# Performance work log

Measured on AMD Instinct MI355X. Metric: run time of the kernel, lower is better.

## Reference

```python
import jax, jax.numpy as jnp
import numpy as np

B, S, E, H = 4, 2048, 1024, 16
D = E // H

def setup_inputs() -> dict:
    key = jax.random.key(0)
    ks = jax.random.split(key, 8)
    sc = lambda fan_in: 1.0 / np.sqrt(fan_in)
    return {
        "query": jax.random.normal(ks[0], (B, S, E), jnp.float32),
        "Wq": jax.random.normal(ks[1], (E, E), jnp.float32) * sc(E),
        "bq": jnp.zeros((E,), jnp.float32),
        "Wk": jax.random.normal(ks[2], (E, E), jnp.float32) * sc(E),
        "bk": jnp.zeros((E,), jnp.float32),
        "Wv": jax.random.normal(ks[3], (E, E), jnp.float32) * sc(E),
        "bv": jnp.zeros((E,), jnp.float32),
        "Wo": jax.random.normal(ks[4], (E, E), jnp.float32) * sc(E),
        "bo": jnp.zeros((E,), jnp.float32),
        "Wm1": jax.random.normal(ks[5], (E // 4, E), jnp.float32) * sc(E),
        "bm1": jnp.zeros((E // 4,), jnp.float32),
        "Wm2": jax.random.normal(ks[6], (E, E // 4), jnp.float32) * sc(E // 4),
        "bm2": jnp.zeros((E,), jnp.float32),
        "dopamine": jnp.ones((1,), jnp.float32),
        "serotonin": jnp.ones((1,), jnp.float32),
        "norepinephrine": jnp.ones((1,), jnp.float32),
        "acetylcholine": jnp.ones((1,), jnp.float32),
        "attn_scale": jnp.ones((1,), jnp.float32),
        "attn_bias": jnp.zeros((1,), jnp.float32),
    }

def reference(query, Wq, bq, Wk, bk, Wv, bv, Wo, bo,
              Wm1, bm1, Wm2, bm2,
              dopamine, serotonin, norepinephrine, acetylcholine,
              attn_scale, attn_bias):
    scale = D ** (-0.5)
    # projections (nn.Linear: y = x @ W.T + b)
    q = (query @ Wq.T + bq).reshape(B, S, H, D).transpose(0, 2, 1, 3)  # [B,H,S,D]
    k = (query @ Wk.T + bk).reshape(B, S, H, D).transpose(0, 2, 1, 3)
    v = (query @ Wv.T + bv).reshape(B, S, H, D).transpose(0, 2, 1, 3)
    scores = jnp.einsum('bhqd,bhkd->bhqk', q, k) * scale  # [B,H,S,S]
    probs = jax.nn.softmax(scores, axis=-1)
    attn = jnp.einsum('bhqk,bhkd->bhqd', probs, v)  # [B,H,S,D]
    # neuromodulation: MLP on query, summed scalar-weighted effects / 4
    mod = jax.nn.relu(query @ Wm1.T + bm1) @ Wm2.T + bm2  # [B,S,E]
    nm_gain = (dopamine + serotonin + norepinephrine + acetylcholine) / 4.0  # [1]
    neuromod = (mod * nm_gain).reshape(B, S, H, D).transpose(0, 2, 1, 3)  # [B,H,S,D]
    attn = (attn * attn_scale + attn_bias) * (1.0 + neuromod)
    attn = attn.transpose(0, 2, 1, 3).reshape(B, S, E)
    return attn @ Wo.T + bo
```

## Files before the change

kernel.cpp:

```cpp
#include <hip/hip_runtime.h>
#include <hip/hip_bf16.h>
#include <cstdint>

#define PB 4
#define PS 2048
#define PE 1024
#define PH 16
#define PD 64
#define PM (PB * PS)

typedef __attribute__((ext_vector_type(8))) _Float16 half8;
typedef __attribute__((ext_vector_type(4))) float f32x4;

#define MFMAH __builtin_amdgcn_mfma_f32_16x16x32_f16

#define GLOAD_LDS(gp, lp) __builtin_amdgcn_global_load_lds(                    \
    (const __attribute__((address_space(1))) void*)(gp),                       \
    (__attribute__((address_space(3))) void*)(lp), 16, 0, 0)

#if __has_builtin(__builtin_amdgcn_exp2f)
#define FAST_EXP2 1
#define QSC (0.125f * 1.4426950408889634f)
#define FTHR 11.5415603f
#define EXP_P(x) __builtin_amdgcn_exp2f(x)
#else
#define FAST_EXP2 0
#define QSC 0.125f
#define FTHR 8.f
#define EXP_P(x) __expf(x)
#endif

__device__ inline unsigned short h16(float x) {
    _Float16 h = (_Float16)x;
    unsigned short u;
    __builtin_memcpy(&u, &h, 2);
    return u;
}
__device__ inline unsigned pkrtz(float a, float b) {
    auto p = __builtin_amdgcn_cvt_pkrtz(a, b);
    unsigned u;
    __builtin_memcpy(&u, &p, 4);
    return u;
}

__global__ __launch_bounds__(256)
void split_all(const float* __restrict__ q,   const float* __restrict__ wq,
               const float* __restrict__ wk,  const float* __restrict__ wv,
               const float* __restrict__ wo,  const float* __restrict__ wm1,
               const float* __restrict__ wm2,
               unsigned short* qh,  unsigned short* wqh, unsigned short* wkh,
               unsigned short* wvh, unsigned short* woh,
               unsigned short* m1h, unsigned short* m2h)
{
    const int b = blockIdx.x;
    const float* src; unsigned short* dst; int base;
    if      (b <  8192) { src = q;   dst = qh;  base = 0;     }
    else if (b <  9216) { src = wq;  dst = wqh; base = 8192;  }
    else if (b < 10240) { src = wk;  dst = wkh; base = 9216;  }
    else if (b < 11264) { src = wv;  dst = wvh; base = 10240; }
    else if (b < 12288) { src = wo;  dst = woh; base = 11264; }
    else if (b < 12544) { src = wm1; dst = m1h; base = 12288; }
    else                { src = wm2; dst = m2h; base = 12544; }
    const int i = (b - base) * 256 + threadIdx.x;
    float4 f = ((const float4*)src)[i];
    ushort4 h;
    h.x = h16(f.x); h.y = h16(f.y); h.z = h16(f.z); h.w = h16(f.w);
    ((ushort4*)dst)[i] = h;
}

__global__ __launch_bounds__(512, 2)
void gemm_qkv(const unsigned short* __restrict__ Ah,
              const unsigned short* __restrict__ Wqh,
              const unsigned short* __restrict__ Wkh,
              const unsigned short* __restrict__ Wvh,
              const float* __restrict__ bq, const float* __restrict__ bk,
              const float* __restrict__ bv,
              unsigned short* __restrict__ qh16, unsigned short* __restrict__ kf,
              unsigned short* __restrict__ vtf)
{
    __shared__ int4 ldsq[8192];
    char* const lds = (char*)ldsq;
    const int K = PE;

    const int tid  = threadIdx.x;
    const int lane = tid & 63;
    const int w    = tid >> 6;
    const int lq   = lane & 15;
    const int lg   = lane >> 4;
    const int wr   = w >> 2;
    const int wc   = w & 3;
    const int m0   = blockIdx.x * 128;
    const int n0   = blockIdx.y * 128;

    const int plane = w >> 1;
    const unsigned short* const gp =
        (plane == 0) ? Ah  + (size_t)m0 * K :
        (plane == 1) ? Wqh + (size_t)n0 * K :
        (plane == 2) ? Wkh + (size_t)n0 * K :
                       Wvh + (size_t)n0 * K;
    const int pbase = plane * 16384;
    const int ch0   = (w & 1) * 8;
    const int scol8 = (((lane & 7) ^ (lane >> 3)) << 3);
    const int lrow8 = lane >> 3;

    auto ISSUE = [&](int k0, int bufn) {
        #pragma unroll
        for (int r = 0; r < 8; ++r) {
            const int c   = ch0 + r;
            const int row = c * 8 + lrow8;
            GLOAD_LDS(gp + (size_t)row * K + k0 + scol8,
                      lds + bufn * 65536 + pbase + c * 1024 + 16 * lane);
        }
    };

    f32x4 acc[3][4][2];
    #pragma unroll
    for (int o = 0; o < 3; ++o)
        #pragma unroll
        for (int mt = 0; mt < 4; ++mt)
            #pragma unroll
            for (int nt = 0; nt < 2; ++nt)
                acc[o][mt][nt] = (f32x4){0.f, 0.f, 0.f, 0.f};

    ISSUE(0, 0);
    __syncthreads();

    int buf = 0;
    for (int k0 = 0; k0 < K; k0 += 64) {
        if (k0 + 64 < K) ISSUE(k0 + 64, buf ^ 1);

        const char* const L = lds + buf * 65536;
        #pragma unroll
        for (int kh = 0; kh < 2; ++kh) {
            half8 af[4];
            #pragma unroll
            for (int mt = 0; mt < 4; ++mt) {
                const int row = 64 * wr + 16 * mt + lq;
                const int off = row * 128 + ((kh * 64 + 16 * lg) ^ ((row & 7) << 4));
                af[mt] = *(const half8*)(L + off);
            }
            #pragma unroll
            for (int o = 0; o < 3; ++o) {
                #pragma unroll
                for (int nt = 0; nt < 2; ++nt) {
                    const int row = 32 * wc + 16 * nt + lq;
                    const int off = row * 128 + ((kh * 64 + 16 * lg) ^ ((row & 7) << 4));
                    half8 bf = *(const half8*)(L + 16384 * (o + 1) + off);
                    #pragma unroll
                    for (int mt = 0; mt < 4; ++mt)
                        acc[o][mt][nt] = MFMAH(af[mt], bf, acc[o][mt][nt], 0, 0, 0);
                }
            }
        }
        __syncthreads();
        buf ^= 1;
    }

    #pragma unroll
    for (int nt = 0; nt < 2; ++nt) {
        const int n = n0 + 32 * wc + 16 * nt + lq;
        const int h = n >> 6, d = n & 63;
        const float bqv = bq[n], bkv = bk[n], bvv = bv[n];
        #pragma unroll
        for (int mt = 0; mt < 4; ++mt) {
            #pragma unroll
            for (int j = 0; j < 4; ++j) {
                const int m = m0 + 64 * wr + 16 * mt + 4 * lg + j;
                const int b = m >> 11, s = m & 2047;
                qh16[((size_t)(b * PH + h) * PS + s) * PD + d] =
                    h16((acc[0][mt][nt][j] + bqv) * QSC);
                kf[((size_t)(b * PH + h) * PS + s) * PD + d] =
                    h16(acc[1][mt][nt][j] + bkv);
                const int scol = (s & ~63) + ((mt & 1) << 5) + (lg << 3)
                               + ((mt >> 1) << 2) + j;
                vtf[((size_t)(b * PH + h) * PD + d) * PS + scol] =
                    h16(acc[2][mt][nt][j] + bvv);
            }
        }
    }
}

template<int MODE, bool RELU>
__global__ __launch_bounds__(256, 2)
void gemm_pl(const unsigned short* __restrict__ Ah,
             const unsigned short* __restrict__ Bh,
             const float* __restrict__ bias, float* __restrict__ C,
             unsigned short* __restrict__ Oh,
             int M, int N, int K,
             const float* __restrict__ attn,
             const float* __restrict__ g0, const float* __restrict__ g1,
             const float* __restrict__ g2, const float* __restrict__ g3,
             const float* __restrict__ asc, const float* __restrict__ abi)
{
    __shared__ int4 ldsq[4096];
    char* const lds = (char*)ldsq;

    const int tid  = threadIdx.x;
    const int lane = tid & 63;
    const int w    = tid >> 6;
    const int lq   = lane & 15;
    const int lg   = lane >> 4;
    const int wm   = (w >> 1) * 64;
    const int wn   = (w & 1) * 64;
    const int m0   = blockIdx.x * 128;
    const int n0   = blockIdx.y * 128;

    const unsigned short* const gp =
        (w < 2) ? Ah + (size_t)m0 * K : Bh + (size_t)n0 * K;
    const int pb    = (w < 2) ? 0 : 16384;
    const int ch0   = (w & 1) * 8;
    const int scol8 = (((lane & 7) ^ (lane >> 3)) << 3);
    const int lrow8 = lane >> 3;

    auto ISSUE = [&](int k0, int bufn) {
        #pragma unroll
        for (int r = 0; r < 8; ++r) {
            const int c   = ch0 + r;
            const int row = c * 8 + lrow8;
            GLOAD_LDS(gp + (size_t)row * K + k0 + scol8,
                      lds + bufn * 32768 + pb + c * 1024 + 16 * lane);
        }
    };

    f32x4 acc[4][4];
    #pragma unroll
    for (int mt = 0; mt < 4; ++mt)
        #pragma unroll
        for (int nt = 0; nt < 4; ++nt)
            acc[mt][nt] = (f32x4){0.f, 0.f, 0.f, 0.f};

    ISSUE(0, 0);
    __syncthreads();

    int buf = 0;
    for (int k0 = 0; k0 < K; k0 += 64) {
        if (k0 + 64 < K) ISSUE(k0 + 64, buf ^ 1);

        const char* const L = lds + buf * 32768;
        #pragma unroll
        for (int kh = 0; kh < 2; ++kh) {
            half8 af[4];
            #pragma unroll
            for (int mt = 0; mt < 4; ++mt) {
                const int row = wm + 16 * mt + lq;
                const int off = row * 128 + ((kh * 64 + 16 * lg) ^ ((row & 7) << 4));
                af[mt] = *(const half8*)(L + off);
            }
            #pragma unroll
            for (int nt = 0; nt < 4; ++nt) {
                const int row = wn + 16 * nt + lq;
                const int off = row * 128 + ((kh * 64 + 16 * lg) ^ ((row & 7) << 4));
                half8 bf = *(const half8*)(L + 16384 + off);
                #pragma unroll
                for (int mt = 0; mt < 4; ++mt)
                    acc[mt][nt] = MFMAH(af[mt], bf, acc[mt][nt], 0, 0, 0);
            }
        }
        __syncthreads();
        buf ^= 1;
    }

    float gain = 0.f, ascv = 0.f, abiv = 0.f;
    if (MODE == 6) {
        gain = 0.25f * (*g0 + *g1 + *g2 + *g3);
        ascv = *asc;
        abiv = *abi;
    }

    #pragma unroll
    for (int nt = 0; nt < 4; ++nt) {
        const int n  = n0 + wn + 16 * nt + lq;
        const float bv = bias[n];
        #pragma unroll
        for (int mt = 0; mt < 4; ++mt) {
            #pragma unroll
            for (int j = 0; j < 4; ++j) {
                const int m = m0 + wm + 16 * mt + 4 * lg + j;
                float v = acc[mt][nt][j] + bv;
                if (RELU) v = fmaxf(v, 0.f);
                if (MODE == 0) {
                    C[(size_t)m * N + n] = v;
                } else if (MODE == 5) {
                    Oh[(size_t)m * N + n] = h16(v);
                } else {
                    const int b = m >> 11, s = m & 2047;
                    const int h = n >> 6, d = n & 63;
                    const float av = attn[((size_t)(b * PH + h) * PS + s) * PD + d];
                    const float o = (av * ascv + abiv) * (1.f + v * gain);
                    Oh[(size_t)m * N + n] = h16(o);
                }
            }
        }
    }
}

typedef __attribute__((ext_vector_type(8))) short short8;
#define MFMA16 __builtin_amdgcn_mfma_f32_16x16x32_bf16
__device__ inline unsigned short bf16rn(float x) {
    unsigned u = __builtin_bit_cast(unsigned, x);
    u += 0x7FFFu + ((u >> 16) & 1u);
    return (unsigned short)(u >> 16);
}
__device__ inline float bf16tof(unsigned short h) {
    unsigned u = ((unsigned)h) << 16;
    return __builtin_bit_cast(float, u);
}
__device__ inline void split2(float x, unsigned short& h, unsigned short& l) {
    h = bf16rn(x);
    l = bf16rn(x - bf16tof(h));
}

template<int MODE, bool RELU>
__global__ __launch_bounds__(256, 2)
void gemm_nt(const float* __restrict__ A, const float* __restrict__ Bw,
             const float* __restrict__ bias, float* __restrict__ C,
             unsigned short* __restrict__ Ohi,
             int M, int N, int K,
             const float* __restrict__ attn,
             const float* __restrict__ g0, const float* __restrict__ g1,
             const float* __restrict__ g2, const float* __restrict__ g3,
             const float* __restrict__ asc, const float* __restrict__ abi)
{
    __shared__ int4 ldsq[4096];
    char* const lds = (char*)ldsq;

    const int tid  = threadIdx.x;
    const int lane = tid & 63;
    const int w    = tid >> 6;
    const int lq   = lane & 15;
    const int lg   = lane >> 4;
    const int wm   = (w >> 1) * 64;
    const int wn   = (w & 1) * 64;
    const int m0   = blockIdx.x * 128;
    const int n0   = blockIdx.y * 128;

    const int irow = tid >> 3;
    const int ic8  = (tid & 7) * 8;
    const int woff = (ic8 * 2);

    f32x4 acc[4][4];
    #pragma unroll
    for (int mt = 0; mt < 4; ++mt)
        #pragma unroll
        for (int nt = 0; nt < 4; ++nt)
            acc[mt][nt] = (f32x4){0.f, 0.f, 0.f, 0.f};

    for (int k0 = 0; k0 < K; k0 += 64) {
        #pragma unroll
        for (int mat = 0; mat < 2; ++mat) {
            const float* const src = mat ? Bw : A;
            const int rbase = mat ? n0 : m0;
            const int pbase = mat ? 32768 : 0;
            #pragma unroll
            for (int r = 0; r < 4; ++r) {
                const int row = irow + 32 * r;
                const float* p = src + (size_t)(rbase + row) * K + k0 + ic8;
                float4 f0 = *(const float4*)p;
                float4 f1 = *(const float4*)(p + 4);
                short8 vh, vl;
                {
                    unsigned short h, l;
                    split2(f0.x, h, l); vh[0] = (short)h; vl[0] = (short)l;
                    split2(f0.y, h, l); vh[1] = (short)h; vl[1] = (short)l;
                    split2(f0.z, h, l); vh[2] = (short)h; vl[2] = (short)l;
                    split2(f0.w, h, l); vh[3] = (short)h; vl[3] = (short)l;
                    split2(f1.x, h, l); vh[4] = (short)h; vl[4] = (short)l;
                    split2(f1.y, h, l); vh[5] = (short)h; vl[5] = (short)l;
                    split2(f1.z, h, l); vh[6] = (short)h; vl[6] = (short)l;
                    split2(f1.w, h, l); vh[7] = (short)h; vl[7] = (short)l;
                }
                const int off = row * 128 + (woff ^ ((row & 7) << 4));
                *(short8*)(lds + pbase + off)         = vh;
                *(short8*)(lds + pbase + 16384 + off) = vl;
            }
        }
        __syncthreads();

        #pragma unroll
        for (int kh = 0; kh < 2; ++kh) {
            short8 afh[4], afl[4];
            #pragma unroll
            for (int mt = 0; mt < 4; ++mt) {
                const int row = wm + 16 * mt + lq;
                const int off = row * 128 + ((kh * 64 + 16 * lg) ^ ((row & 7) << 4));
                afh[mt] = *(const short8*)(lds + off);
                afl[mt] = *(const short8*)(lds + 16384 + off);
            }
            #pragma unroll
            for (int nt = 0; nt < 4; ++nt) {
                const int row = wn + 16 * nt + lq;
                const int off = row * 128 + ((kh * 64 + 16 * lg) ^ ((row & 7) << 4));
                short8 bfh = *(const short8*)(lds + 32768 + off);
                short8 bfl = *(const short8*)(lds + 49152 + off);
                #pragma unroll
                for (int mt = 0; mt < 4; ++mt) {
                    acc[mt][nt] = MFMA16(afh[mt], bfh, acc[mt][nt], 0, 0, 0);
                    acc[mt][nt] = MFMA16(afh[mt], bfl, acc[mt][nt], 0, 0, 0);
                    acc[mt][nt] = MFMA16(afl[mt], bfh, acc[mt][nt], 0, 0, 0);
                }
            }
        }
        __syncthreads();
    }

    float gain = 0.f, ascv = 0.f, abiv = 0.f;
    if (MODE == 2) {
        gain = 0.25f * (*g0 + *g1 + *g2 + *g3);
        ascv = *asc;
        abiv = *abi;
    }

    #pragma unroll
    for (int nt = 0; nt < 4; ++nt) {
        const int n  = n0 + wn + 16 * nt + lq;
        const float bv = bias[n];
        #pragma unroll
        for (int mt = 0; mt < 4; ++mt) {
            #pragma unroll
            for (int j = 0; j < 4; ++j) {
                const int m = m0 + wm + 16 * mt + 4 * lg + j;
                float v = acc[mt][nt][j] + bv;
                if (RELU) v = fmaxf(v, 0.f);
                if (MODE == 0) {
                    C[(size_t)m * N + n] = v;
                } else if (MODE == 1) {
                    const int b = m >> 11, s = m & 2047;
                    const int h = n >> 6, d = n & 63;
                    Ohi[((size_t)(b * PH + h) * PS + s) * PD + d] = h16(v * QSC);
                } else if (MODE == 3) {
                    const int b = m >> 11, s = m & 2047;
                    const int h = n >> 6, d = n & 63;
                    Ohi[((size_t)(b * PH + h) * PS + s) * PD + d] = h16(v);
                } else if (MODE == 4) {
                    const int b = m >> 11;
                    const int h = n >> 6, d = n & 63;
                    const int scol = (m & 2047 & ~63) + ((mt & 1) << 5)
                                   + (lg << 3) + ((mt >> 1) << 2) + j;
                    Ohi[((size_t)(b * PH + h) * PD + d) * PS + scol] = h16(v);
                } else {
                    const int b = m >> 11, s = m & 2047;
                    const int h = n >> 6, d = n & 63;
                    const float av = attn[((size_t)(b * PH + h) * PS + s) * PD + d];
                    C[(size_t)m * N + n] = (av * ascv + abiv) * (1.f + v * gain);
                }
            }
        }
    }
}

__global__ __launch_bounds__(256, 4)
void flash_mfma(const unsigned short* __restrict__ qh16,
                const unsigned short* __restrict__ kf,
                const unsigned short* __restrict__ vtf,
                float* attn)
{
    __shared__ int4 ldsv[2048];
    char* const ldsb = (char*)ldsv;

    const int tid  = threadIdx.x;
    const int lane = tid & 63;
    const int w    = tid >> 6;
    const int lq   = lane & 15;
    const int lg   = lane >> 4;

    const int L  = blockIdx.x + (blockIdx.y << 4) + (blockIdx.z << 8);
    const int nL = ((L & 7) << 7) + (L >> 3);
    const int bh = nL >> 4;
    const int q0 = (nL & 15) * 128 + w * 32;

    const size_t kbase = (size_t)bh * PS * PD;
    const size_t vbase = (size_t)bh * PD * PS;

    const unsigned short* const gp = (w < 2) ? kf + kbase : vtf + vbase;
    const bool isK = (w < 2);
    const int ch0   = (w & 1) * 4;
    const int scol8 = (((lane & 7) ^ (lane >> 3)) << 3);
    const int lrow8 = lane >> 3;

    auto ISSUE = [&](int kt, int bufn) {
        #pragma unroll
        for (int r = 0; r < 4; ++r) {
            const int c   = ch0 + r;
            const int row = c * 8 + lrow8;
            const size_t goff = isK ? (size_t)(kt + row) * PD + scol8
                                    : (size_t)row * PS + kt + scol8;
            GLOAD_LDS(gp + goff,
                      ldsb + bufn * 16384 + (isK ? 0 : 8192) + c * 1024 + 16 * lane);
        }
    };

    const half8 onesh = {(_Float16)1.f, (_Float16)1.f, (_Float16)1.f,
                         (_Float16)1.f, (_Float16)1.f, (_Float16)1.f,
                         (_Float16)1.f, (_Float16)1.f};

    half8 qh[2][2];
    #pragma unroll
    for (int u = 0; u < 2; ++u) {
        const unsigned short* qp =
            qh16 + ((size_t)bh * PS + q0 + 16 * u + lq) * PD + 8 * lg;
        qh[u][0] = *(const half8*)(qp);
        qh[u][1] = *(const half8*)(qp + 32);
    }

    f32x4 ot[2][4];
    #pragma unroll
    for (int u = 0; u < 2; ++u)
        #pragma unroll
        for (int mt = 0; mt < 4; ++mt)
            ot[u][mt] = (f32x4){0.f, 0.f, 0.f, 0.f};
    f32x4 lacc[2] = {{0.f,0.f,0.f,0.f}, {0.f,0.f,0.f,0.f}};
    float m_run[2] = {-3.0e38f, -3.0e38f};

    ISSUE(0, 0);
    __syncthreads();

    int buf = 0;
    for (int kti = 0; kti < PS / 64; ++kti) {
        const bool pf = (kti + 1 < PS / 64);
        if (pf) ISSUE((kti + 1) * 64, buf ^ 1);

        const char* const L2 = ldsb + buf * 16384;

        f32x4 st[2][4];
        #pragma unroll
        for (int mt = 0; mt < 4; ++mt) {
            const int row = 16 * mt + lq;
            const int swz = (row & 7) << 4;
            const char* kr = L2 + row * 128;
            half8 a0 = *(const half8*)(kr + ((16 * lg) ^ swz));
            half8 a1 = *(const half8*)(kr + ((64 + 16 * lg) ^ swz));
            #pragma unroll
            for (int u = 0; u < 2; ++u) {
                f32x4 acc = {0.f, 0.f, 0.f, 0.f};
                acc = MFMAH(a0, qh[u][0], acc, 0, 0, 0);
                acc = MFMAH(a1, qh[u][1], acc, 0, 0, 0);
                st[u][mt] = acc;
            }
        }

        half8 pb[2][2];
        #pragma unroll
        for (int u = 0; u < 2; ++u) {
            float a0 = fmaxf(fmaxf(st[u][0][0], st[u][0][1]), st[u][0][2]);
            float a1 = fmaxf(fmaxf(st[u][0][3], st[u][1][0]), st[u][1][1]);
            float a2 = fmaxf(fmaxf(st[u][1][2], st[u][1][3]), st[u][2][0]);
            float a3 = fmaxf(fmaxf(st[u][2][1], st[u][2][2]), st[u][2][3]);
            float a4 = fmaxf(fmaxf(st[u][3][0], st[u][3][1]), st[u][3][2]);
            float b0 = fmaxf(fmaxf(a0, a1), a2);
            float b1 = fmaxf(fmaxf(a3, a4), st[u][3][3]);
            float pmax = fmaxf(b0, b1);
            pmax = fmaxf(pmax, __shfl_xor(pmax, 16));
            pmax = fmaxf(pmax, __shfl_xor(pmax, 32));
            if (!__all(pmax - m_run[u] <= FTHR)) {
                float mnew = fmaxf(m_run[u], pmax);
                float corr = EXP_P(m_run[u] - mnew);
                m_run[u] = mnew;
                #pragma unroll
                for (int j = 0; j < 4; ++j)
                    lacc[u][j] *= corr;
                #pragma unroll
                for (int mt = 0; mt < 4; ++mt)
                    #pragma unroll
                    for (int j = 0; j < 4; ++j)
                        ot[u][mt][j] *= corr;
            }
            #pragma unroll
            for (int mt = 0; mt < 4; ++mt)
                #pragma unroll
                for (int j = 0; j < 4; ++j)
                    st[u][mt][j] = EXP_P(st[u][mt][j] - m_run[u]);
            #pragma unroll
            for (int t = 0; t < 2; ++t) {
                unsigned w0 = pkrtz(st[u][t][0],     st[u][t][1]);
                unsigned w1 = pkrtz(st[u][t][2],     st[u][t][3]);
                unsigned w2 = pkrtz(st[u][t + 2][0], st[u][t + 2][1]);
                unsigned w3 = pkrtz(st[u][t + 2][2], st[u][t + 2][3]);
                uint4 pw = make_uint4(w0, w1, w2, w3);
                __builtin_memcpy(&pb[u][t], &pw, 16);
            }
            lacc[u] = MFMAH(onesh, pb[u][0], lacc[u], 0, 0, 0);
            lacc[u] = MFMAH(onesh, pb[u][1], lacc[u], 0, 0, 0);
        }

        #pragma unroll
        for (int t = 0; t < 2; ++t) {
            #pragma unroll
            for (int mt = 0; mt < 4; ++mt) {
                const int row = 16 * mt + lq;
                const int swz = (row & 7) << 4;
                const char* vr = L2 + 8192 + row * 128;
                half8 vv = *(const half8*)(vr + ((t * 64 + 16 * lg) ^ swz));
                #pragma unroll
                for (int u = 0; u < 2; ++u)
                    ot[u][mt] = MFMAH(vv, pb[u][t], ot[u][mt], 0, 0, 0);
            }
        }

        __syncthreads();
        buf ^= 1;
    }

    #pragma unroll
    for (int u = 0; u < 2; ++u) {
        const float inv = 1.f / lacc[u][0];
        float* op = attn + ((size_t)bh * PS + q0 + 16 * u + lq) * PD + 4 * lg;
        #pragma unroll
        for (int mt = 0; mt < 4; ++mt) {
            float4 o;
            o.x = ot[u][mt][0] * inv; o.y = ot[u][mt][1] * inv;
            o.z = ot[u][mt][2] * inv; o.w = ot[u][mt][3] * inv;
            *(float4*)(op + 16 * mt) = o;
        }
    }
}

extern "C" void kernel_launch(void* const* d_in, const int* in_sizes, int n_in,
                              void* d_out, int out_size, void* d_ws, size_t ws_size,
                              hipStream_t stream)
{
    const float* query = (const float*)d_in[0];
    const float* Wq  = (const float*)d_in[1];  const float* bq  = (const float*)d_in[2];
    const float* Wk  = (const float*)d_in[3];  const float* bk  = (const float*)d_in[4];
    const float* Wv  = (const float*)d_in[5];  const float* bv  = (const float*)d_in[6];
    const float* Wo  = (const float*)d_in[7];  const float* bo  = (const float*)d_in[8];
    const float* Wm1 = (const float*)d_in[9];  const float* bm1 = (const float*)d_in[10];
    const float* Wm2 = (const float*)d_in[11]; const float* bm2 = (const float*)d_in[12];
    const float* dop = (const float*)d_in[13];
    const float* ser = (const float*)d_in[14];
    const float* nor = (const float*)d_in[15];
    const float* ach = (const float*)d_in[16];
    const float* asc = (const float*)d_in[17];
    const float* abi = (const float*)d_in[18];
    float* out = (float*)d_out;

    char* wsb = (char*)d_ws;
    float*          attnb = (float*)wsb;
    unsigned short* kf    = (unsigned short*)(wsb + (32u << 20));
    unsigned short* vtf   = (unsigned short*)(wsb + (48u << 20));

    dim3 blk(256);
    const bool presplit = (ws_size >= 161480704ull);

    if (presplit) {
        unsigned short* h1h   = (unsigned short*)(wsb + (64u << 20));
        unsigned short* afh   = (unsigned short*)(wsb + (72u << 20));
        unsigned short* qh16  = (unsigned short*)(wsb + (88u << 20));
        unsigned short* qh    = (unsigned short*)(wsb + (104u << 20));
        unsigned short* wqh   = (unsigned short*)(wsb + (136u << 20));
        unsigned short* wkh   = (unsigned short*)(wsb + (138u << 20));
        unsigned short* wvh   = (unsigned short*)(wsb + (140u << 20));
        unsigned short* woh   = (unsigned short*)(wsb + (142u << 20));
        unsigned short* m1h   = (unsigned short*)(wsb + (144u << 20));
        unsigned short* m2h   = (unsigned short*)(wsb + (145u << 20));

        split_all<<<12800, blk, 0, stream>>>(
            query, Wq, Wk, Wv, Wo, Wm1, Wm2,
            qh, wqh, wkh, wvh, woh, m1h, m2h);

        gemm_qkv<<<dim3(PM / 128, PE / 128), dim3(512), 0, stream>>>(
            qh, wqh, wkh, wvh, bq, bk, bv, qh16, kf, vtf);

        gemm_pl<5, true><<<dim3(PM / 128, 256 / 128), blk, 0, stream>>>(
            qh, m1h, bm1, nullptr, h1h, PM, 256, PE,
            nullptr, nullptr, nullptr, nullptr, nullptr, nullptr, nullptr);

        flash_mfma<<<dim3(PS / 128, PH, PB), blk, 0, stream>>>(
            qh16, kf, vtf, attnb);

        gemm_pl<6, false><<<dim3(PM / 128, PE / 128), blk, 0, stream>>>(
            h1h, m2h, bm2, nullptr, afh, PM, PE, 256,
            attnb, dop, ser, nor, ach, asc, abi);
        gemm_pl<0, false><<<dim3(PM / 128, PE / 128), blk, 0, stream>>>(
            afh, woh, bo, out, nullptr, PM, PE, PE,
            nullptr, nullptr, nullptr, nullptr, nullptr, nullptr, nullptr);
    } else {
        float* h1    = (float*)(wsb + (64u << 20));
        float* attnf = (float*)(wsb + (72u << 20));
        unsigned short* qh16 = (unsigned short*)(wsb + (72u << 20));

        gemm_nt<1, false><<<dim3(PM / 128, PE / 128), blk, 0, stream>>>(
            query, Wq, bq, nullptr, qh16, PM, PE, PE,
            nullptr, nullptr, nullptr, nullptr, nullptr, nullptr, nullptr);
        gemm_nt<3, false><<<dim3(PM / 128, PE / 128), blk, 0, stream>>>(
            query, Wk, bk, nullptr, kf, PM, PE, PE,
            nullptr, nullptr, nullptr, nullptr, nullptr, nullptr, nullptr);
        gemm_nt<4, false><<<dim3(PM / 128, PE / 128), blk, 0, stream>>>(
            query, Wv, bv, nullptr, vtf, PM, PE, PE,
            nullptr, nullptr, nullptr, nullptr, nullptr, nullptr, nullptr);
        gemm_nt<0, true><<<dim3(PM / 128, 256 / 128), blk, 0, stream>>>(
            query, Wm1, bm1, h1, nullptr, PM, 256, PE,
            nullptr, nullptr, nullptr, nullptr, nullptr, nullptr, nullptr);

        flash_mfma<<<dim3(PS / 128, PH, PB), blk, 0, stream>>>(
            qh16, kf, vtf, attnb);

        gemm_nt<2, false><<<dim3(PM / 128, PE / 128), blk, 0, stream>>>(
            h1, Wm2, bm2, attnf, nullptr, PM, PE, 256,
            attnb, dop, ser, nor, ach, asc, abi);
        gemm_nt<0, false><<<dim3(PM / 128, PE / 128), blk, 0, stream>>>(
            attnf, Wo, bo, out, nullptr, PM, PE, PE,
            nullptr, nullptr, nullptr, nullptr, nullptr, nullptr, nullptr);
    }
}
```

Before: 213.6 us.

## Fuse neuromodulation epilogue into flash attention and emit fp16 modulation

The modulation MLP's second GEMM now writes its output as fp16 to a new buffer. The flash attention kernel applies the scale, bias and neuromodulation gain in its epilogue and writes the fp16 combined activation directly in [B,S,E] layout. This removes the fp32 attention intermediate and its scattered re-read from the GEMM epilogue, cutting global memory traffic. The cost is extra epilogue work and strided reads in the flash kernel, plus fp16 rounding of the modulation values.

```diff
diff --git a/kernel.cpp b/kernel.cpp
--- a/kernel.cpp
+++ b/kernel.cpp
@@ -35,6 +35,11 @@
     unsigned short u;
     __builtin_memcpy(&u, &h, 2);
     return u;
+}
+__device__ inline float f16tof(unsigned short u) {
+    _Float16 h;
+    __builtin_memcpy(&h, &u, 2);
+    return (float)h;
 }
 __device__ inline unsigned pkrtz(float a, float b) {
     auto p = __builtin_amdgcn_cvt_pkrtz(a, b);
@@ -186,11 +191,7 @@
              const unsigned short* __restrict__ Bh,
              const float* __restrict__ bias, float* __restrict__ C,
              unsigned short* __restrict__ Oh,
-             int M, int N, int K,
-             const float* __restrict__ attn,
-             const float* __restrict__ g0, const float* __restrict__ g1,
-             const float* __restrict__ g2, const float* __restrict__ g3,
-             const float* __restrict__ asc, const float* __restrict__ abi)
+             int M, int N, int K)
 {
     __shared__ int4 ldsq[4096];
     char* const lds = (char*)ldsq;
@@ -260,13 +261,6 @@
         buf ^= 1;
     }
 
-    float gain = 0.f, ascv = 0.f, abiv = 0.f;
-    if (MODE == 6) {
-        gain = 0.25f * (*g0 + *g1 + *g2 + *g3);
-        ascv = *asc;
-        abiv = *abi;
-    }
-
     #pragma unroll
     for (int nt = 0; nt < 4; ++nt) {
         const int n  = n0 + wn + 16 * nt + lq;
@@ -280,14 +274,8 @@
                 if (RELU) v = fmaxf(v, 0.f);
                 if (MODE == 0) {
                     C[(size_t)m * N + n] = v;
-                } else if (MODE == 5) {
+                } else {
                     Oh[(size_t)m * N + n] = h16(v);
-                } else {
-                    const int b = m >> 11, s = m & 2047;
-                    const int h = n >> 6, d = n & 63;
-                    const float av = attn[((size_t)(b * PH + h) * PS + s) * PD + d];
-                    const float o = (av * ascv + abiv) * (1.f + v * gain);
-                    Oh[(size_t)m * N + n] = h16(o);
                 }
             }
         }
@@ -448,11 +436,16 @@
     }
 }
 
+template<int FUSE>
 __global__ __launch_bounds__(256, 4)
 void flash_mfma(const unsigned short* __restrict__ qh16,
                 const unsigned short* __restrict__ kf,
                 const unsigned short* __restrict__ vtf,
-                float* attn)
+                const unsigned short* __restrict__ modh,
+                const float* __restrict__ g0, const float* __restrict__ g1,
+                const float* __restrict__ g2, const float* __restrict__ g3,
+                const float* __restrict__ asc, const float* __restrict__ abi,
+                unsigned short* __restrict__ afh, float* __restrict__ attn)
 {
     __shared__ int4 ldsv[2048];
     char* const ldsb = (char*)ldsv;
@@ -600,16 +593,39 @@
         buf ^= 1;
     }
 
-    #pragma unroll
-    for (int u = 0; u < 2; ++u) {
-        const float inv = 1.f / lacc[u][0];
-        float* op = attn + ((size_t)bh * PS + q0 + 16 * u + lq) * PD + 4 * lg;
-        #pragma unroll
-        for (int mt = 0; mt < 4; ++mt) {
-            float4 o;
-            o.x = ot[u][mt][0] * inv; o.y = ot[u][mt][1] * inv;
-            o.z = ot[u][mt][2] * inv; o.w = ot[u][mt][3] * inv;
-            *(float4*)(op + 16 * mt) = o;
+    if (FUSE) {
+        const float gain = 0.25f * (*g0 + *g1 + *g2 + *g3);
+        const float ascv = *asc, abiv = *abi;
+        const int bb = bh >> 4, hh = bh & 15;
+        #pragma unroll
+        for (int u = 0; u < 2; ++u) {
+            const int m = bb * PS + q0 + 16 * u + lq;
+            const unsigned short* mp = modh + (size_t)m * PE + hh * 64 + 4 * lg;
+            unsigned short* op = afh + (size_t)m * PE + hh * 64 + 4 * lg;
+            const float inv = 1.f / lacc[u][0];
+            #pragma unroll
+            for (int mt = 0; mt < 4; ++mt) {
+                ushort4 mv = *(const ushort4*)(mp + 16 * mt);
+                ushort4 ov;
+                ov.x = h16((ot[u][mt][0] * inv * ascv + abiv) * (1.f + f16tof(mv.x) * gain));
+                ov.y = h16((ot[u][mt][1] * inv * ascv + abiv) * (1.f + f16tof(mv.y) * gain));
+                ov.z = h16((ot[u][mt][2] * inv * ascv + abiv) * (1.f + f16tof(mv.z) * gain));
+                ov.w = h16((ot[u][mt][3] * inv * ascv + abiv) * (1.f + f16tof(mv.w) * gain));
+                *(ushort4*)(op + 16 * mt) = ov;
+            }
+        }
+    } else {
+        #pragma unroll
+        for (int u = 0; u < 2; ++u) {
+            const float inv = 1.f / lacc[u][0];
+            float* op = attn + ((size_t)bh * PS + q0 + 16 * u + lq) * PD + 4 * lg;
+            #pragma unroll
+            for (int mt = 0; mt < 4; ++mt) {
+                float4 o;
+                o.x = ot[u][mt][0] * inv; o.y = ot[u][mt][1] * inv;
+                o.z = ot[u][mt][2] * inv; o.w = ot[u][mt][3] * inv;
+                *(float4*)(op + 16 * mt) = o;
+            }
         }
     }
 }
@@ -646,6 +662,7 @@
         unsigned short* afh   = (unsigned short*)(wsb + (72u << 20));
         unsigned short* qh16  = (unsigned short*)(wsb + (88u << 20));
         unsigned short* qh    = (unsigned short*)(wsb + (104u << 20));
+        unsigned short* modh  = (unsigned short*)(wsb + (120u << 20));
         unsigned short* wqh   = (unsigned short*)(wsb + (136u << 20));
         unsigned short* wkh   = (unsigned short*)(wsb + (138u << 20));
         unsigned short* wvh   = (unsigned short*)(wsb + (140u << 20));
@@ -661,18 +678,16 @@
             qh, wqh, wkh, wvh, bq, bk, bv, qh16, kf, vtf);
 
         gemm_pl<5, true><<<dim3(PM / 128, 256 / 128), blk, 0, stream>>>(
-            qh, m1h, bm1, nullptr, h1h, PM, 256, PE,
-            nullptr, nullptr, nullptr, nullptr, nullptr, nullptr, nullptr);
-
-        flash_mfma<<<dim3(PS / 128, PH, PB), blk, 0, stream>>>(
-            qh16, kf, vtf, attnb);
-
-        gemm_pl<6, false><<<dim3(PM / 128, PE / 128), blk, 0, stream>>>(
-            h1h, m2h, bm2, nullptr, afh, PM, PE, 256,
-            attnb, dop, ser, nor, ach, asc, abi);
+            qh, m1h, bm1, nullptr, h1h, PM, 256, PE);
+        gemm_pl<5, false><<<dim3(PM / 128, PE / 128), blk, 0, stream>>>(
+            h1h, m2h, bm2, nullptr, modh, PM, PE, 256);
+
+        flash_mfma<1><<<dim3(PS / 128, PH, PB), blk, 0, stream>>>(
+            qh16, kf, vtf, modh, dop, ser, nor, ach, asc, abi,
+            afh, nullptr);
+
         gemm_pl<0, false><<<dim3(PM / 128, PE / 128), blk, 0, stream>>>(
-            afh, woh, bo, out, nullptr, PM, PE, PE,
-            nullptr, nullptr, nullptr, nullptr, nullptr, nullptr, nullptr);
+            afh, woh, bo, out, nullptr, PM, PE, PE);
     } else {
         float* h1    = (float*)(wsb + (64u << 20));
         float* attnf = (float*)(wsb + (72u << 20));
@@ -691,8 +706,9 @@
             query, Wm1, bm1, h1, nullptr, PM, 256, PE,
             nullptr, nullptr, nullptr, nullptr, nullptr, nullptr, nullptr);
 
-        flash_mfma<<<dim3(PS / 128, PH, PB), blk, 0, stream>>>(
-            qh16, kf, vtf, attnb);
+        flash_mfma<0><<<dim3(PS / 128, PH, PB), blk, 0, stream>>>(
+            qh16, kf, vtf, nullptr, nullptr, nullptr, nullptr, nullptr,
+            nullptr, nullptr, nullptr, attnb);
 
         gemm_nt<2, false><<<dim3(PM / 128, PE / 128), blk, 0, stream>>>(
             h1, Wm2, bm2, attnf, nullptr, PM, PE, 256,
```

Result: faster. 207.7 us (-2.8%).
